# Kernel tuning notes

Measured on AMD Instinct MI355X. Metric: run time of the kernel, lower is better.

## Reference

```python
import jax, jax.numpy as jnp
import numpy as np

NB_VARS = 2_000_000
N0 = 2 + 2 * NB_VARS      # input vector length: [zero, one, pos0, neg0, pos1, neg1, ...]
M0 = 4_000_000            # prod layer 0 outputs (binary fan-in)
M1 = 1_000_000            # sum  layer 1 outputs (irregular fan-in)
M2 = 500_000              # prod layer 2 outputs (binary fan-in)
M3 = 125_000              # sum  layer 3 outputs (irregular fan-in)


def setup_inputs() -> dict:
    key = jax.random.key(0)
    ks = jax.random.split(key, 7)
    x_pos = jax.random.uniform(ks[0], (NB_VARS,), dtype=jnp.float32)
    ix_in0 = jax.random.randint(ks[1], (2 * M0,), 0, N0)            # edges of prod layer 0
    ix_in1 = jax.random.randint(ks[2], (8_000_000,), 0, M0)         # edges of sum layer 1
    ix_out1 = jnp.sort(jax.random.randint(ks[3], (8_000_000,), 0, M1))
    ix_in2 = jax.random.randint(ks[4], (2 * M2,), 0, M1)            # edges of prod layer 2
    ix_in3 = jax.random.randint(ks[5], (1_000_000,), 0, M2)         # edges of sum layer 3
    ix_out3 = jnp.sort(jax.random.randint(ks[6], (1_000_000,), 0, M3))
    return {"x_pos": x_pos, "ix_in0": ix_in0, "ix_in1": ix_in1, "ix_out1": ix_out1,
            "ix_in2": ix_in2, "ix_in3": ix_in3, "ix_out3": ix_out3}


def reference(x_pos, ix_in0, ix_in1, ix_out1, ix_in2, ix_in3, ix_out3):
    # encode_input (real semiring): neg = negate(pos) = 1 - pos; interleave; prepend [zero=0, one=1]
    neg = 1.0 - x_pos
    units = jnp.array([0.0, 1.0], dtype=x_pos.dtype)
    x = jnp.concatenate([units, jnp.stack([x_pos, neg], axis=1).reshape(-1)])  # [N0]

    # layer 0: product layer, binary fan-in -> gather + pairwise multiply
    e0 = x[ix_in0].reshape(M0, 2)
    x = e0[:, 0] * e0[:, 1]                                                    # [M0]

    # layer 1: sum layer, irregular fan-in -> gather + segment-sum
    x = jax.ops.segment_sum(x[ix_in1], ix_out1, num_segments=M1)               # [M1]

    # layer 2: product layer, binary fan-in
    e2 = x[ix_in2].reshape(M2, 2)
    x = e2[:, 0] * e2[:, 1]                                                    # [M2]

    # layer 3: sum layer, irregular fan-in
    x = jax.ops.segment_sum(x[ix_in3], ix_out3, num_segments=M3)               # [M3]
    return x
```

## Files before the change

kernel.cpp:

```cpp
#include <hip/hip_runtime.h>
#include <hip/hip_fp16.h>


#define PERS_BLOCKS 2048
#define PERS_THREADS 256
#define WBITS_F16 21

typedef __attribute__((ext_vector_type(4))) int iv4;

__device__ __forceinline__ iv4 nt_load4(const int* p) {
    return __builtin_nontemporal_load((const iv4*)p);
}

__global__ void cvt16_kernel(const float4* __restrict__ in,
                             uint2* __restrict__ out, int n4) {
    int t = blockIdx.x * blockDim.x + threadIdx.x;
    if (t >= n4) return;
    float4 f = in[t];
    __half2 lo = __floats2half2_rn(f.x, f.y);
    __half2 hi = __floats2half2_rn(f.z, f.w);
    uint2 r;
    r.x = *(const unsigned int*)&lo;
    r.y = *(const unsigned int*)&hi;
    out[t] = r;
}

__device__ __forceinline__ float decode16(const __half* __restrict__ xp, int idx) {
    int k = (idx - 2) >> 1;
    k = k < 0 ? 0 : k;
    float v = __half2float(xp[k]);
    v = (idx & 1) ? 1.0f - v : v;
    if (idx < 2) v = (float)idx;
    return v;
}

__global__ void layer0_prod8_kernel(const __half* __restrict__ x16,
                                    const int* __restrict__ ix,
                                    uint4* __restrict__ out16, int nT) {
    int t = blockIdx.x * blockDim.x + threadIdx.x;
    if (t >= nT) return;
    iv4 p0 = nt_load4(ix + 16 * t);
    iv4 p1 = nt_load4(ix + 16 * t + 4);
    iv4 p2 = nt_load4(ix + 16 * t + 8);
    iv4 p3 = nt_load4(ix + 16 * t + 12);
    float a0 = decode16(x16, p0.x), b0 = decode16(x16, p0.y);
    float a1 = decode16(x16, p0.z), b1 = decode16(x16, p0.w);
    float a2 = decode16(x16, p1.x), b2 = decode16(x16, p1.y);
    float a3 = decode16(x16, p1.z), b3 = decode16(x16, p1.w);
    float a4 = decode16(x16, p2.x), b4 = decode16(x16, p2.y);
    float a5 = decode16(x16, p2.z), b5 = decode16(x16, p2.w);
    float a6 = decode16(x16, p3.x), b6 = decode16(x16, p3.y);
    float a7 = decode16(x16, p3.z), b7 = decode16(x16, p3.w);
    __half2 h0 = __floats2half2_rn(a0 * b0, a1 * b1);
    __half2 h1 = __floats2half2_rn(a2 * b2, a3 * b3);
    __half2 h2 = __floats2half2_rn(a4 * b4, a5 * b5);
    __half2 h3 = __floats2half2_rn(a6 * b6, a7 * b7);
    uint4 r;
    r.x = *(const unsigned int*)&h0;
    r.y = *(const unsigned int*)&h1;
    r.z = *(const unsigned int*)&h2;
    r.w = *(const unsigned int*)&h3;
    out16[t] = r;
}

template<int NS, int NWIN>
__global__ __launch_bounds__(PERS_THREADS)
void sum_win_h_kernel(const __half* __restrict__ vin,
                      const int* __restrict__ ix_in,
                      const int* __restrict__ ix_out,
                      float* __restrict__ out, int nT4) {
    const int nTh  = gridDim.x * blockDim.x;
    const int gtid = blockIdx.x * blockDim.x + threadIdx.x;
    const int lane = threadIdx.x & 63;

    iv4    a[NS];
    iv4    sg[NS];
    float4 v[NS];
    bool   act[NS];
    #pragma unroll
    for (int s = 0; s < NS; ++s) {
        int t = s * nTh + gtid;
        act[s] = (t < nT4);
        if (act[s]) {
            a[s]  = nt_load4(ix_in  + 4 * t);
            sg[s] = nt_load4(ix_out + 4 * t);
        } else {
            a[s]  = (iv4){-1, -1, -1, -1};
            sg[s] = (iv4){-1, -1, -1, -1};
        }
        v[s] = make_float4(0.f, 0.f, 0.f, 0.f);
    }

    #pragma unroll
    for (int w = 0; w < NWIN; ++w) {
        #pragma unroll
        for (int s = 0; s < NS; ++s) {
            if ((a[s].x >> WBITS_F16) == w) v[s].x = __half2float(vin[a[s].x]);
            if ((a[s].y >> WBITS_F16) == w) v[s].y = __half2float(vin[a[s].y]);
            if ((a[s].z >> WBITS_F16) == w) v[s].z = __half2float(vin[a[s].z]);
            if ((a[s].w >> WBITS_F16) == w) v[s].w = __half2float(vin[a[s].w]);
        }
    }

    #pragma unroll
    for (int s = 0; s < NS; ++s) {
        int seg = -1; float val = 0.f;
        if (act[s]) {
            int cur = sg[s].x; float acc = v[s].x;
            if (sg[s].y == cur) acc += v[s].y; else { atomicAdd(&out[cur], acc); cur = sg[s].y; acc = v[s].y; }
            if (sg[s].z == cur) acc += v[s].z; else { atomicAdd(&out[cur], acc); cur = sg[s].z; acc = v[s].z; }
            if (sg[s].w == cur) acc += v[s].w; else { atomicAdd(&out[cur], acc); cur = sg[s].w; acc = v[s].w; }
            seg = cur; val = acc;
        }
        #pragma unroll
        for (int off = 1; off < 64; off <<= 1) {
            float vv = __shfl_up(val, off, 64);
            int   ss = __shfl_up(seg, off, 64);
            if (lane >= off && ss == seg) val += vv;
        }
        int seg_next = __shfl_down(seg, 1, 64);
        bool is_last = (lane == 63) || (seg_next != seg);
        if (act[s] && is_last) atomicAdd(&out[seg], val);
    }
}

__global__ void sum4_f32_kernel(const float* __restrict__ vin,
                                const int* __restrict__ ix_in,
                                const int* __restrict__ ix_out,
                                float* __restrict__ out, int nT4) {
    int t = blockIdx.x * blockDim.x + threadIdx.x;
    int lane = threadIdx.x & 63;
    int seg = -1; float val = 0.f;
    if (t < nT4) {
        iv4 a  = nt_load4(ix_in  + 4 * t);
        iv4 sg = nt_load4(ix_out + 4 * t);
        float v0 = vin[a.x], v1 = vin[a.y], v2 = vin[a.z], v3 = vin[a.w];
        int cur = sg.x; float acc = v0;
        if (sg.y == cur) acc += v1; else { atomicAdd(&out[cur], acc); cur = sg.y; acc = v1; }
        if (sg.z == cur) acc += v2; else { atomicAdd(&out[cur], acc); cur = sg.z; acc = v2; }
        if (sg.w == cur) acc += v3; else { atomicAdd(&out[cur], acc); cur = sg.w; acc = v3; }
        seg = cur; val = acc;
    }
    #pragma unroll
    for (int off = 1; off < 64; off <<= 1) {
        float vv = __shfl_up(val, off, 64);
        int   ss = __shfl_up(seg, off, 64);
        if (lane >= off && ss == seg) val += vv;
    }
    int seg_next = __shfl_down(seg, 1, 64);
    bool is_last = (lane == 63) || (seg_next != seg);
    if (t < nT4 && is_last) atomicAdd(&out[seg], val);
}

__global__ void prod2_kernel(const float* __restrict__ vin,
                             const int* __restrict__ ix,
                             float2* __restrict__ out, int nT) {
    int t = blockIdx.x * blockDim.x + threadIdx.x;
    if (t >= nT) return;
    iv4 p = nt_load4(ix + 4 * t);
    float a0 = vin[p.x], b0 = vin[p.y];
    float a1 = vin[p.z], b1 = vin[p.w];
    float2 r; r.x = a0 * b0; r.y = a1 * b1;
    out[t] = r;
}

extern "C" void kernel_launch(void* const* d_in, const int* in_sizes, int n_in,
                              void* d_out, int out_size, void* d_ws, size_t ws_size,
                              hipStream_t stream) {
    const float* x_pos  = (const float*)d_in[0];
    const int*   ix_in0 = (const int*)d_in[1];
    const int*   ix_in1 = (const int*)d_in[2];
    const int*   ix_out1= (const int*)d_in[3];
    const int*   ix_in2 = (const int*)d_in[4];
    const int*   ix_in3 = (const int*)d_in[5];
    const int*   ix_out3= (const int*)d_in[6];
    float* out = (float*)d_out;

    const int NV = in_sizes[0];
    const int M0 = in_sizes[1] / 2;
    const int E1 = in_sizes[2];
    const int M1 = 1000000;
    const int M2 = in_sizes[4] / 2;
    const int E3 = in_sizes[5];
    const int M3 = out_size;

    char* ws = (char*)d_ws;
    __half* y0  = (__half*)(ws);
    float*  y1  = (float*)(ws + (size_t)8  * 1024 * 1024);
    float*  y2  = (float*)(ws + (size_t)12 * 1024 * 1024);
    __half* x16 = (__half*)(ws + (size_t)14 * 1024 * 1024);

    hipMemsetAsync(y1,  0, (size_t)M1 * sizeof(float), stream);
    hipMemsetAsync(out, 0, (size_t)M3 * sizeof(float), stream);

    const int B = 256;

    int nc = NV / 4;
    cvt16_kernel<<<(nc + B - 1) / B, B, 0, stream>>>(
        (const float4*)x_pos, (uint2*)x16, nc);

    int t0 = M0 / 8;
    layer0_prod8_kernel<<<(t0 + B - 1) / B, B, 0, stream>>>(
        x16, ix_in0, (uint4*)y0, t0);

    int t1 = E1 / 4;
    sum_win_h_kernel<4, 2><<<PERS_BLOCKS, PERS_THREADS, 0, stream>>>(
        y0, ix_in1, ix_out1, y1, t1);

    int t2 = M2 / 2;
    prod2_kernel<<<(t2 + B - 1) / B, B, 0, stream>>>(
        y1, ix_in2, (float2*)y2, t2);

    int t3 = E3 / 4;
    sum4_f32_kernel<<<(t3 + B - 1) / B, B, 0, stream>>>(
        y2, ix_in3, ix_out3, out, t3);
}
```

Before: 257.8 us.

## Fuse memsets into fp16 conversion kernel, use nontemporal stores, narrow gather windows

The two hipMemsetAsync calls and the fp16 conversion kernel are merged into a single init kernel that also zeroes the y1 and output accumulators, which removes launch overhead. Layer 0 now writes its fp16 output with nontemporal stores, and index arithmetic is widened to size_t. The windowed gather in the layer-1 sum kernel uses four 2MB windows instead of two 4MB windows, aiming for better cache locality in exchange for more passes over the predicated loads. The init kernel relies on M1 and M3 being divisible by 4 and on the conversion grid covering the zeroing ranges.

```diff
diff --git a/kernel.cpp b/kernel.cpp
--- a/kernel.cpp
+++ b/kernel.cpp
@@ -4,25 +4,37 @@
 
 #define PERS_BLOCKS 2048
 #define PERS_THREADS 256
-#define WBITS_F16 21
-
-typedef __attribute__((ext_vector_type(4))) int iv4;
+#define WBITS_H 20
+
+typedef __attribute__((ext_vector_type(4))) int   iv4;
+typedef __attribute__((ext_vector_type(4))) float fv4;
+typedef __attribute__((ext_vector_type(4))) unsigned int uv4;
 
 __device__ __forceinline__ iv4 nt_load4(const int* p) {
     return __builtin_nontemporal_load((const iv4*)p);
 }
 
-__global__ void cvt16_kernel(const float4* __restrict__ in,
-                             uint2* __restrict__ out, int n4) {
-    int t = blockIdx.x * blockDim.x + threadIdx.x;
-    if (t >= n4) return;
-    float4 f = in[t];
-    __half2 lo = __floats2half2_rn(f.x, f.y);
-    __half2 hi = __floats2half2_rn(f.z, f.w);
-    uint2 r;
-    r.x = *(const unsigned int*)&lo;
-    r.y = *(const unsigned int*)&hi;
-    out[t] = r;
+__global__ void init_kernel(const float* __restrict__ in, unsigned int* __restrict__ x16,
+                            float* __restrict__ y1, float* __restrict__ out,
+                            int n4, int nz1, int nzo) {
+    int t = blockIdx.x * blockDim.x + threadIdx.x;
+    if (t < n4) {
+        fv4 f = __builtin_nontemporal_load((const fv4*)(in + 4 * (size_t)t));
+        __half2 lo = __floats2half2_rn(f.x, f.y);
+        __half2 hi = __floats2half2_rn(f.z, f.w);
+        unsigned int rlo = *(const unsigned int*)&lo;
+        unsigned int rhi = *(const unsigned int*)&hi;
+        x16[2 * t]     = rlo;
+        x16[2 * t + 1] = rhi;
+    }
+    if (t < nz1) {
+        fv4 z = {0.f, 0.f, 0.f, 0.f};
+        __builtin_nontemporal_store(z, (fv4*)(y1 + 4 * (size_t)t));
+    }
+    if (t < nzo) {
+        fv4 z = {0.f, 0.f, 0.f, 0.f};
+        __builtin_nontemporal_store(z, (fv4*)(out + 4 * (size_t)t));
+    }
 }
 
 __device__ __forceinline__ float decode16(const __half* __restrict__ xp, int idx) {
@@ -36,13 +48,13 @@
 
 __global__ void layer0_prod8_kernel(const __half* __restrict__ x16,
                                     const int* __restrict__ ix,
-                                    uint4* __restrict__ out16, int nT) {
+                                    unsigned int* __restrict__ out16, int nT) {
     int t = blockIdx.x * blockDim.x + threadIdx.x;
     if (t >= nT) return;
-    iv4 p0 = nt_load4(ix + 16 * t);
-    iv4 p1 = nt_load4(ix + 16 * t + 4);
-    iv4 p2 = nt_load4(ix + 16 * t + 8);
-    iv4 p3 = nt_load4(ix + 16 * t + 12);
+    iv4 p0 = nt_load4(ix + 16 * (size_t)t);
+    iv4 p1 = nt_load4(ix + 16 * (size_t)t + 4);
+    iv4 p2 = nt_load4(ix + 16 * (size_t)t + 8);
+    iv4 p3 = nt_load4(ix + 16 * (size_t)t + 12);
     float a0 = decode16(x16, p0.x), b0 = decode16(x16, p0.y);
     float a1 = decode16(x16, p0.z), b1 = decode16(x16, p0.w);
     float a2 = decode16(x16, p1.x), b2 = decode16(x16, p1.y);
@@ -55,12 +67,12 @@
     __half2 h1 = __floats2half2_rn(a2 * b2, a3 * b3);
     __half2 h2 = __floats2half2_rn(a4 * b4, a5 * b5);
     __half2 h3 = __floats2half2_rn(a6 * b6, a7 * b7);
-    uint4 r;
+    uv4 r;
     r.x = *(const unsigned int*)&h0;
     r.y = *(const unsigned int*)&h1;
     r.z = *(const unsigned int*)&h2;
     r.w = *(const unsigned int*)&h3;
-    out16[t] = r;
+    __builtin_nontemporal_store(r, (uv4*)(out16 + 4 * (size_t)t));
 }
 
 template<int NS, int NWIN>
@@ -82,8 +94,8 @@
         int t = s * nTh + gtid;
         act[s] = (t < nT4);
         if (act[s]) {
-            a[s]  = nt_load4(ix_in  + 4 * t);
-            sg[s] = nt_load4(ix_out + 4 * t);
+            a[s]  = nt_load4(ix_in  + 4 * (size_t)t);
+            sg[s] = nt_load4(ix_out + 4 * (size_t)t);
         } else {
             a[s]  = (iv4){-1, -1, -1, -1};
             sg[s] = (iv4){-1, -1, -1, -1};
@@ -95,10 +107,10 @@
     for (int w = 0; w < NWIN; ++w) {
         #pragma unroll
         for (int s = 0; s < NS; ++s) {
-            if ((a[s].x >> WBITS_F16) == w) v[s].x = __half2float(vin[a[s].x]);
-            if ((a[s].y >> WBITS_F16) == w) v[s].y = __half2float(vin[a[s].y]);
-            if ((a[s].z >> WBITS_F16) == w) v[s].z = __half2float(vin[a[s].z]);
-            if ((a[s].w >> WBITS_F16) == w) v[s].w = __half2float(vin[a[s].w]);
+            if ((a[s].x >> WBITS_H) == w) v[s].x = __half2float(vin[a[s].x]);
+            if ((a[s].y >> WBITS_H) == w) v[s].y = __half2float(vin[a[s].y]);
+            if ((a[s].z >> WBITS_H) == w) v[s].z = __half2float(vin[a[s].z]);
+            if ((a[s].w >> WBITS_H) == w) v[s].w = __half2float(vin[a[s].w]);
         }
     }
 
@@ -132,8 +144,8 @@
     int lane = threadIdx.x & 63;
     int seg = -1; float val = 0.f;
     if (t < nT4) {
-        iv4 a  = nt_load4(ix_in  + 4 * t);
-        iv4 sg = nt_load4(ix_out + 4 * t);
+        iv4 a  = nt_load4(ix_in  + 4 * (size_t)t);
+        iv4 sg = nt_load4(ix_out + 4 * (size_t)t);
         float v0 = vin[a.x], v1 = vin[a.y], v2 = vin[a.z], v3 = vin[a.w];
         int cur = sg.x; float acc = v0;
         if (sg.y == cur) acc += v1; else { atomicAdd(&out[cur], acc); cur = sg.y; acc = v1; }
@@ -157,7 +169,7 @@
                              float2* __restrict__ out, int nT) {
     int t = blockIdx.x * blockDim.x + threadIdx.x;
     if (t >= nT) return;
-    iv4 p = nt_load4(ix + 4 * t);
+    iv4 p = nt_load4(ix + 4 * (size_t)t);
     float a0 = vin[p.x], b0 = vin[p.y];
     float a1 = vin[p.z], b1 = vin[p.w];
     float2 r; r.x = a0 * b0; r.y = a1 * b1;
@@ -190,21 +202,20 @@
     float*  y2  = (float*)(ws + (size_t)12 * 1024 * 1024);
     __half* x16 = (__half*)(ws + (size_t)14 * 1024 * 1024);
 
-    hipMemsetAsync(y1,  0, (size_t)M1 * sizeof(float), stream);
-    hipMemsetAsync(out, 0, (size_t)M3 * sizeof(float), stream);
-
     const int B = 256;
 
-    int nc = NV / 4;
-    cvt16_kernel<<<(nc + B - 1) / B, B, 0, stream>>>(
-        (const float4*)x_pos, (uint2*)x16, nc);
+    int n4  = NV / 4;
+    int nz1 = M1 / 4;
+    int nzo = M3 / 4;
+    init_kernel<<<(n4 + B - 1) / B, B, 0, stream>>>(
+        x_pos, (unsigned int*)x16, y1, out, n4, nz1, nzo);
 
     int t0 = M0 / 8;
     layer0_prod8_kernel<<<(t0 + B - 1) / B, B, 0, stream>>>(
-        x16, ix_in0, (uint4*)y0, t0);
+        x16, ix_in0, (unsigned int*)y0, t0);
 
     int t1 = E1 / 4;
-    sum_win_h_kernel<4, 2><<<PERS_BLOCKS, PERS_THREADS, 0, stream>>>(
+    sum_win_h_kernel<4, 4><<<PERS_BLOCKS, PERS_THREADS, 0, stream>>>(
         y0, ix_in1, ix_out1, y1, t1);
 
     int t2 = M2 / 2;
```

Measured after the change: 252.6 us. 1.02x faster.
